# Optimization experiments

Measured on AMD Instinct MI355X. Metric: run time of the kernel, lower is better.

The kernel has to match this reference:

```python
import jax, jax.numpy as jnp
import numpy as np

B, S, DMODEL, HEADS = 2, 2048, 1024, 16
DK = DMODEL // HEADS
DV = DMODEL // HEADS


def setup_inputs() -> dict:
    key = jax.random.key(0)
    kx, kq, kk, kv = jax.random.split(key, 4)
    x = jax.random.normal(kx, (B, S, DMODEL), dtype=jnp.float32)
    # stacked per-head projection weights, shape [H, dmodel, dk/dv]
    # (equivalent to nn.Linear(dmodel, dk, bias=False) per head)
    scale = 1.0 / np.sqrt(DMODEL)
    Wq = jax.random.uniform(kq, (HEADS, DMODEL, DK), jnp.float32, -scale, scale)
    Wk = jax.random.uniform(kk, (HEADS, DMODEL, DK), jnp.float32, -scale, scale)
    Wv = jax.random.uniform(kv, (HEADS, DMODEL, DV), jnp.float32, -scale, scale)
    return {"x": x, "Wq": Wq, "Wk": Wk, "Wv": Wv}


def reference(x, Wq, Wk, Wv):
    # per-head projections, batched across heads: [B,H,S,dk]
    q = jnp.einsum("bsd,hdk->bhsk", x, Wq)
    k = jnp.einsum("bsd,hdk->bhsk", x, Wk)
    v = jnp.einsum("bsd,hdv->bhsv", x, Wv)
    # NOTE: original module applies NO 1/sqrt(dk) scaling — keep faithful
    scores = jnp.einsum("bhqk,bhsk->bhqs", q, k)  # [B,H,S,S]
    attn = jax.nn.softmax(scores, axis=-1)
    out = jnp.einsum("bhqs,bhsv->bhqv", attn, v)  # [B,H,S,dv]
    # concat heads along last dim in head order
    Bsz, H, Sq, Dv = out.shape
    return jnp.transpose(out, (0, 2, 1, 3)).reshape(Bsz, Sq, H * Dv)
```

## Files before the change

### kernel.cpp

```cpp
#include <hip/hip_runtime.h>

#define B_ 2
#define S_ 2048
#define D_ 1024
#define H_ 16
#define DK_ 64
#define M_ (B_ * S_)
#define N_ (3 * D_)

typedef __bf16 bf16x8 __attribute__((ext_vector_type(8)));
typedef short s8vec __attribute__((ext_vector_type(8)));
typedef float f4vec __attribute__((ext_vector_type(4)));

static __device__ __forceinline__ ushort f2b(float f) {
  union { float f; unsigned u; } v; v.f = f;
  unsigned u = v.u;
  u += 0x7FFFu + ((u >> 16) & 1u);
  return (ushort)(u >> 16);
}

static __device__ __forceinline__ unsigned pk2(float a, float b) {
#if __has_builtin(__builtin_amdgcn_cvt_pk_bf16_f32)
  typedef __bf16 b2 __attribute__((ext_vector_type(2)));
  b2 r = __builtin_amdgcn_cvt_pk_bf16_f32(a, b);
  return __builtin_bit_cast(unsigned, r);
#else
  return (unsigned)f2b(a) | ((unsigned)f2b(b) << 16);
#endif
}

static __device__ __forceinline__ float fexp2(float x) {
#if __has_builtin(__builtin_amdgcn_exp2f)
  return __builtin_amdgcn_exp2f(x);
#else
  return exp2f(x);
#endif
}

static __device__ __forceinline__ f4vec mfma16(s8vec a, s8vec b, f4vec c) {
  return __builtin_amdgcn_mfma_f32_16x16x32_bf16(
      __builtin_bit_cast(bf16x8, a), __builtin_bit_cast(bf16x8, b), c, 0, 0, 0);
}

static __device__ __forceinline__ void gl_lds16(const ushort* g, ushort* l) {
  __builtin_amdgcn_global_load_lds(
      (const __attribute__((address_space(1))) unsigned*)g,
      (__attribute__((address_space(3))) unsigned*)l, 16, 0, 0);
}

static __device__ __forceinline__ void wg_barrier_lds() {
  asm volatile("" ::: "memory");
  __builtin_amdgcn_s_waitcnt(0xC07F);
  __builtin_amdgcn_s_barrier();
  asm volatile("" ::: "memory");
}

__global__ void cvt_x(const float* __restrict__ x, ushort* __restrict__ xb) {
  int i = blockIdx.x * 256 + threadIdx.x;
  float4 v = ((const float4*)x)[i];
  ushort4 o;
  o.x = f2b(v.x); o.y = f2b(v.y); o.z = f2b(v.z); o.w = f2b(v.w);
  ((ushort4*)xb)[i] = o;
}

__global__ __launch_bounds__(256) void cvt_w(const float* __restrict__ Wq,
                                             const float* __restrict__ Wk,
                                             const float* __restrict__ Wv,
                                             ushort* __restrict__ wbt) {
  __shared__ ushort T[64 * 72];
  const int w = blockIdx.z, h = blockIdx.y, d0 = blockIdx.x * 64;
  const float* W = (w == 0) ? Wq : (w == 1) ? Wk : Wv;
  const float* src = W + (size_t)h * 65536 + (size_t)d0 * 64;
  const int t = threadIdx.x;
#pragma unroll
  for (int j = 0; j < 4; ++j) {
    int idx = j * 256 + t;
    int dr = idx >> 4, kc = (idx & 15) * 4;
    float4 v = *(const float4*)(src + dr * 64 + kc);
    T[(kc + 0) * 72 + dr] = f2b(v.x);
    T[(kc + 1) * 72 + dr] = f2b(v.y);
    T[(kc + 2) * 72 + dr] = f2b(v.z);
    T[(kc + 3) * 72 + dr] = f2b(v.w);
  }
  __syncthreads();
  const int kk = t >> 2, dcg = (t & 3) * 16;
  ushort* dst = wbt + ((size_t)w * 1024 + h * 64 + kk) * 1024 + d0 + dcg;
  *(s8vec*)dst       = *(const s8vec*)&T[kk * 72 + dcg];
  *(s8vec*)(dst + 8) = *(const s8vec*)&T[kk * 72 + dcg + 8];
}

__global__ __launch_bounds__(256) void proj_gemm(const ushort* __restrict__ xb,
                                                 const ushort* __restrict__ wbt,
                                                 ushort* __restrict__ qkv) {
  __shared__ __attribute__((aligned(16))) ushort As[128 * 64];
  __shared__ __attribute__((aligned(16))) ushort Bs[128 * 64];
  const int tid = threadIdx.x, wid = tid >> 6, lane = tid & 63;
  const int quad = lane >> 4, l15 = lane & 15;
  const int wm = wid & 1, wn = wid >> 1;
  const int m0 = blockIdx.x * 128, n0 = blockIdx.y * 128;

  f4vec acc[4][4];
#pragma unroll
  for (int mb = 0; mb < 4; mb++)
#pragma unroll
    for (int nb = 0; nb < 4; nb++)
#pragma unroll
      for (int i = 0; i < 4; i++) acc[mb][nb][i] = 0.f;

  const int sr = tid >> 3, sg = tid & 7;
  const int lg = sg ^ (sr & 7);
  const ushort* Ab = xb + (size_t)m0 * D_;
  const ushort* Bb = wbt + (size_t)n0 * D_;

  for (int k0 = 0; k0 < D_; k0 += 64) {
    __syncthreads();
#pragma unroll
    for (int j = 0; j < 4; ++j) {
      int r = j * 32 + sr;
      gl_lds16(Ab + (size_t)r * D_ + k0 + lg * 8, &As[j * 2048 + wid * 512]);
      gl_lds16(Bb + (size_t)r * D_ + k0 + lg * 8, &Bs[j * 2048 + wid * 512]);
    }
    __syncthreads();

#pragma unroll
    for (int kb = 0; kb < 2; ++kb) {
      s8vec af[4], bf[4];
#pragma unroll
      for (int mb = 0; mb < 4; ++mb) {
        int m = wm * 64 + mb * 16 + l15;
        int gpos = (kb * 4 + quad) ^ (m & 7);
        af[mb] = *(const s8vec*)&As[m * 64 + gpos * 8];
      }
#pragma unroll
      for (int nb = 0; nb < 4; ++nb) {
        int n = wn * 64 + nb * 16 + l15;
        int gpos = (kb * 4 + quad) ^ (n & 7);
        bf[nb] = *(const s8vec*)&Bs[n * 64 + gpos * 8];
      }
#pragma unroll
      for (int mb = 0; mb < 4; ++mb)
#pragma unroll
        for (int nb = 0; nb < 4; ++nb)
          acc[mb][nb] = mfma16(af[mb], bf[nb], acc[mb][nb]);
    }
  }

  const size_t per = (size_t)B_ * H_ * S_ * DK_;
  const int w = n0 >> 10;
  if (w == 2) {
    ushort* vt = qkv + 2 * per;
#pragma unroll
    for (int mb = 0; mb < 4; ++mb)
#pragma unroll
      for (int nb = 0; nb < 4; ++nb)
#pragma unroll
        for (int i = 0; i < 4; ++i) {
          int m = m0 + wm * 64 + mb * 16 + quad * 4 + i;
          int b = m >> 11, s = m & 2047;
          int n1 = (n0 & 1023) + wn * 64 + nb * 16 + l15;
          vt[((size_t)b * 1024 + n1) * S_ + s] = f2b(acc[mb][nb][i]);
        }
  } else {
    const float qs = (w == 0) ? 1.44269504f : 1.0f;
#pragma unroll
    for (int mb = 0; mb < 4; ++mb)
#pragma unroll
      for (int nb = 0; nb < 4; ++nb)
#pragma unroll
        for (int i = 0; i < 4; ++i) {
          int m = m0 + wm * 64 + mb * 16 + quad * 4 + i;
          int b = m >> 11, s = m & 2047;
          int n1 = (n0 & 1023) + wn * 64 + nb * 16 + l15;
          qkv[(size_t)w * per + (((size_t)b * H_ + (n1 >> 6)) * S_ + s) * 64 + (n1 & 63)] =
              f2b(acc[mb][nb][i] * qs);
        }
  }
}

__global__ __launch_bounds__(256) void attn(const ushort* __restrict__ qg,
                                            const ushort* __restrict__ kg,
                                            const ushort* __restrict__ vtg,
                                            float* __restrict__ out) {
  __shared__ __attribute__((aligned(16))) ushort Ks[128 * 64];
  __shared__ __attribute__((aligned(16))) ushort Vt[2][64 * 64];
  __shared__ __attribute__((aligned(16))) ushort Ps[4][32 * 132];
  const int qt = blockIdx.x, bh = blockIdx.y;
  const int b = bh >> 4, h = bh & 15;
  const int tid = threadIdx.x, wid = tid >> 6, lane = tid & 63;
  const int quad = lane >> 4, l15 = lane & 15, l7 = l15 & 7;

  const ushort* qbase = qg + ((size_t)bh * S_ + qt * 128 + wid * 32) * DK_;
  s8vec aq[2][2];
#pragma unroll
  for (int mb = 0; mb < 2; mb++) {
    aq[mb][0] = *(const s8vec*)(qbase + (size_t)(mb * 16 + l15) * DK_ + quad * 8);
    aq[mb][1] = *(const s8vec*)(qbase + (size_t)(mb * 16 + l15) * DK_ + 32 + quad * 8);
  }

  f4vec o[2][4];
  float lsum[2][4];
#pragma unroll
  for (int mb = 0; mb < 2; mb++)
#pragma unroll
    for (int i = 0; i < 4; i++) {
      lsum[mb][i] = 0.f;
#pragma unroll
      for (int nb = 0; nb < 4; nb++) o[mb][nb][i] = 0.f;
    }

  const int r = tid >> 3, gs = tid & 7;
  const int gk = gs ^ (r & 7);
  const ushort* kb_ = kg + (size_t)bh * S_ * DK_;
  const ushort* vb_ = vtg + (size_t)bh * 64 * S_;

  s8vec kpre[4], vpre[4];
#pragma unroll
  for (int j = 0; j < 4; ++j)
    kpre[j] = *(const s8vec*)(kb_ + (size_t)(j * 32 + r) * DK_ + gk * 8);
  vpre[0] = *(const s8vec*)(vb_ + (size_t)r * S_ + gk * 8);
  vpre[1] = *(const s8vec*)(vb_ + (size_t)r * S_ + 64 + gk * 8);
  vpre[2] = *(const s8vec*)(vb_ + (size_t)(r + 32) * S_ + gk * 8);
  vpre[3] = *(const s8vec*)(vb_ + (size_t)(r + 32) * S_ + 64 + gk * 8);

  for (int kt = 0; kt < S_ / 128; ++kt) {
    wg_barrier_lds();
#pragma unroll
    for (int j = 0; j < 4; ++j)
      *(s8vec*)&Ks[(j * 32 + r) * 64 + gs * 8] = kpre[j];
    *(s8vec*)&Vt[0][r * 64 + gs * 8]        = vpre[0];
    *(s8vec*)&Vt[1][r * 64 + gs * 8]        = vpre[1];
    *(s8vec*)&Vt[0][(r + 32) * 64 + gs * 8] = vpre[2];
    *(s8vec*)&Vt[1][(r + 32) * 64 + gs * 8] = vpre[3];
    if (kt + 1 < S_ / 128) {
      const ushort* kn = kb_ + (size_t)((kt + 1) * 128 + r) * DK_ + gk * 8;
#pragma unroll
      for (int j = 0; j < 4; ++j)
        kpre[j] = *(const s8vec*)(kn + (size_t)(j * 32) * DK_);
      const ushort* vn = vb_ + (size_t)r * S_ + (kt + 1) * 128 + gk * 8;
      vpre[0] = *(const s8vec*)(vn);
      vpre[1] = *(const s8vec*)(vn + 64);
      vpre[2] = *(const s8vec*)(vn + (size_t)32 * S_);
      vpre[3] = *(const s8vec*)(vn + (size_t)32 * S_ + 64);
    }
    wg_barrier_lds();

    f4vec sc[2][8];
#pragma unroll
    for (int nb = 0; nb < 8; nb++) {
      const int row = nb * 16 + l15;
      s8vec bk0 = *(const s8vec*)&Ks[row * 64 + ((0 + quad) ^ l7) * 8];
      s8vec bk1 = *(const s8vec*)&Ks[row * 64 + ((4 + quad) ^ l7) * 8];
#pragma unroll
      for (int mb = 0; mb < 2; mb++) {
        f4vec z;
#pragma unroll
        for (int i = 0; i < 4; i++) z[i] = 0.f;
        z = mfma16(aq[mb][0], bk0, z);
        sc[mb][nb] = mfma16(aq[mb][1], bk1, z);
      }
    }

#pragma unroll
    for (int mb = 0; mb < 2; mb++)
#pragma unroll
      for (int nb = 0; nb < 8; nb++) {
#pragma unroll
        for (int i = 0; i < 4; i++) {
          float p = fexp2(sc[mb][nb][i]);
          sc[mb][nb][i] = p;
          lsum[mb][i] += p;
        }
        unsigned p01 = pk2(sc[mb][nb][0], sc[mb][nb][1]);
        unsigned p23 = pk2(sc[mb][nb][2], sc[mb][nb][3]);
        ushort* pw = &Ps[wid][(mb * 16 + quad * 4) * 132 + nb * 16 + l15];
        pw[0]   = (ushort)p01;
        pw[132] = (ushort)(p01 >> 16);
        pw[264] = (ushort)p23;
        pw[396] = (ushort)(p23 >> 16);
      }

#pragma unroll
    for (int kb2 = 0; kb2 < 4; kb2++) {
      s8vec ap0 = *(const s8vec*)(&Ps[wid][(l15) * 132 + kb2 * 32 + quad * 8]);
      s8vec ap1 = *(const s8vec*)(&Ps[wid][(16 + l15) * 132 + kb2 * 32 + quad * 8]);
      const int half = kb2 >> 1, G = (kb2 & 1) * 4 + quad;
#pragma unroll
      for (int nb = 0; nb < 4; nb++) {
        s8vec bv = *(const s8vec*)&Vt[half][(nb * 16 + l15) * 64 + (G ^ l7) * 8];
        o[0][nb] = mfma16(ap0, bv, o[0][nb]);
        o[1][nb] = mfma16(ap1, bv, o[1][nb]);
      }
    }
  }

#pragma unroll
  for (int mb = 0; mb < 2; mb++)
#pragma unroll
    for (int i = 0; i < 4; i++) {
#pragma unroll
      for (int msk = 1; msk < 16; msk <<= 1)
        lsum[mb][i] += __shfl_xor(lsum[mb][i], msk, 64);
    }

#pragma unroll
  for (int mb = 0; mb < 2; mb++) {
    float* ob = out + ((size_t)b * S_ + qt * 128 + wid * 32 + mb * 16) * D_ + h * DK_;
#pragma unroll
    for (int i = 0; i < 4; i++) {
      float inv = 1.0f / lsum[mb][i];
#pragma unroll
      for (int nb = 0; nb < 4; nb++)
        ob[(size_t)(quad * 4 + i) * D_ + nb * 16 + l15] = o[mb][nb][i] * inv;
    }
  }
}

extern "C" void kernel_launch(void* const* d_in, const int* in_sizes, int n_in,
                              void* d_out, int out_size, void* d_ws, size_t ws_size,
                              hipStream_t stream) {
  const float* x  = (const float*)d_in[0];
  const float* Wq = (const float*)d_in[1];
  const float* Wk = (const float*)d_in[2];
  const float* Wv = (const float*)d_in[3];
  float* out = (float*)d_out;

  ushort* xb  = (ushort*)d_ws;
  ushort* wbt = xb + (size_t)B_ * S_ * D_;
  ushort* qkv = wbt + (size_t)3 * D_ * D_;
  const size_t per = (size_t)B_ * H_ * S_ * DK_;

  cvt_x<<<(B_ * S_ * D_) / 4 / 256, 256, 0, stream>>>(x, xb);
  cvt_w<<<dim3(16, 16, 3), 256, 0, stream>>>(Wq, Wk, Wv, wbt);
  proj_gemm<<<dim3(M_ / 128, N_ / 128), 256, 0, stream>>>(xb, wbt, qkv);
  attn<<<dim3(S_ / 128, B_ * H_), 256, 0, stream>>>(qkv, qkv + per, qkv + 2 * per, out);
}
```

Baseline: 176.9 us.

## Transpose attention MFMA operands, halve KV tile, merge conversion kernels

Merges the x and weight bf16 conversion kernels into one launch to save a kernel launch. In attention, it swaps MFMA operand order so each lane holds a full query row's scores. This turns the row-sum reduction into two shuffles, lets P be written as packed 8-byte swizzled stores without row padding, and lets the output be written as float4. The KV tile shrinks from 128 to 64 keys, which cuts LDS use and registers but doubles the number of loop iterations and barriers.

New measurement: 177.5 us. Within noise of the previous version (+0.4%).

```diff
diff --git a/kernel.cpp b/kernel.cpp
--- a/kernel.cpp
+++ b/kernel.cpp
@@ -55,38 +55,42 @@
   asm volatile("" ::: "memory");
 }
 
-__global__ void cvt_x(const float* __restrict__ x, ushort* __restrict__ xb) {
-  int i = blockIdx.x * 256 + threadIdx.x;
-  float4 v = ((const float4*)x)[i];
-  ushort4 o;
-  o.x = f2b(v.x); o.y = f2b(v.y); o.z = f2b(v.z); o.w = f2b(v.w);
-  ((ushort4*)xb)[i] = o;
-}
-
-__global__ __launch_bounds__(256) void cvt_w(const float* __restrict__ Wq,
-                                             const float* __restrict__ Wk,
-                                             const float* __restrict__ Wv,
-                                             ushort* __restrict__ wbt) {
-  __shared__ ushort T[64 * 72];
-  const int w = blockIdx.z, h = blockIdx.y, d0 = blockIdx.x * 64;
-  const float* W = (w == 0) ? Wq : (w == 1) ? Wk : Wv;
-  const float* src = W + (size_t)h * 65536 + (size_t)d0 * 64;
+__global__ __launch_bounds__(256) void cvt_all(const float* __restrict__ x,
+                                               const float* __restrict__ Wq,
+                                               const float* __restrict__ Wk,
+                                               const float* __restrict__ Wv,
+                                               ushort* __restrict__ xb,
+                                               ushort* __restrict__ wbt) {
   const int t = threadIdx.x;
-#pragma unroll
-  for (int j = 0; j < 4; ++j) {
-    int idx = j * 256 + t;
-    int dr = idx >> 4, kc = (idx & 15) * 4;
-    float4 v = *(const float4*)(src + dr * 64 + kc);
-    T[(kc + 0) * 72 + dr] = f2b(v.x);
-    T[(kc + 1) * 72 + dr] = f2b(v.y);
-    T[(kc + 2) * 72 + dr] = f2b(v.z);
-    T[(kc + 3) * 72 + dr] = f2b(v.w);
-  }
-  __syncthreads();
-  const int kk = t >> 2, dcg = (t & 3) * 16;
-  ushort* dst = wbt + ((size_t)w * 1024 + h * 64 + kk) * 1024 + d0 + dcg;
-  *(s8vec*)dst       = *(const s8vec*)&T[kk * 72 + dcg];
-  *(s8vec*)(dst + 8) = *(const s8vec*)&T[kk * 72 + dcg + 8];
+  if (blockIdx.x < 4096) {
+    int i = blockIdx.x * 256 + t;
+    float4 v = ((const float4*)x)[i];
+    ushort4 o;
+    o.x = f2b(v.x); o.y = f2b(v.y); o.z = f2b(v.z); o.w = f2b(v.w);
+    ((ushort4*)xb)[i] = o;
+  } else {
+    __shared__ ushort T[64 * 72];
+    int bid = blockIdx.x - 4096;
+    int w = bid >> 8, rem = bid & 255;
+    int h = rem >> 4, d0 = (rem & 15) * 64;
+    const float* W = (w == 0) ? Wq : (w == 1) ? Wk : Wv;
+    const float* src = W + (size_t)h * 65536 + (size_t)d0 * 64;
+#pragma unroll
+    for (int j = 0; j < 4; ++j) {
+      int idx = j * 256 + t;
+      int dr = idx >> 4, kc = (idx & 15) * 4;
+      float4 v = *(const float4*)(src + dr * 64 + kc);
+      T[(kc + 0) * 72 + dr] = f2b(v.x);
+      T[(kc + 1) * 72 + dr] = f2b(v.y);
+      T[(kc + 2) * 72 + dr] = f2b(v.z);
+      T[(kc + 3) * 72 + dr] = f2b(v.w);
+    }
+    __syncthreads();
+    const int kk = t >> 2, dcg = (t & 3) * 16;
+    ushort* dst = wbt + ((size_t)w * 1024 + h * 64 + kk) * 1024 + d0 + dcg;
+    *(s8vec*)dst       = *(const s8vec*)&T[kk * 72 + dcg];
+    *(s8vec*)(dst + 8) = *(const s8vec*)&T[kk * 72 + dcg + 8];
+  }
 }
 
 __global__ __launch_bounds__(256) void proj_gemm(const ushort* __restrict__ xb,
@@ -181,9 +185,9 @@
                                             const ushort* __restrict__ kg,
                                             const ushort* __restrict__ vtg,
                                             float* __restrict__ out) {
-  __shared__ __attribute__((aligned(16))) ushort Ks[128 * 64];
-  __shared__ __attribute__((aligned(16))) ushort Vt[2][64 * 64];
-  __shared__ __attribute__((aligned(16))) ushort Ps[4][32 * 132];
+  __shared__ __attribute__((aligned(16))) ushort Ks[64 * 64];
+  __shared__ __attribute__((aligned(16))) ushort Vt[64 * 64];
+  __shared__ __attribute__((aligned(16))) ushort Ps[4][32 * 128];
   const int qt = blockIdx.x, bh = blockIdx.y;
   const int b = bh >> 4, h = bh & 15;
   const int tid = threadIdx.x, wid = tid >> 6, lane = tid & 63;
@@ -198,119 +202,110 @@
   }
 
   f4vec o[2][4];
-  float lsum[2][4];
-#pragma unroll
-  for (int mb = 0; mb < 2; mb++)
-#pragma unroll
-    for (int i = 0; i < 4; i++) {
-      lsum[mb][i] = 0.f;
-#pragma unroll
-      for (int nb = 0; nb < 4; nb++) o[mb][nb][i] = 0.f;
-    }
+  float lsum[2];
+#pragma unroll
+  for (int mb = 0; mb < 2; mb++) {
+    lsum[mb] = 0.f;
+#pragma unroll
+    for (int nb = 0; nb < 4; nb++)
+#pragma unroll
+      for (int i = 0; i < 4; i++) o[mb][nb][i] = 0.f;
+  }
 
   const int r = tid >> 3, gs = tid & 7;
   const int gk = gs ^ (r & 7);
   const ushort* kb_ = kg + (size_t)bh * S_ * DK_;
   const ushort* vb_ = vtg + (size_t)bh * 64 * S_;
 
-  s8vec kpre[4], vpre[4];
-#pragma unroll
-  for (int j = 0; j < 4; ++j)
-    kpre[j] = *(const s8vec*)(kb_ + (size_t)(j * 32 + r) * DK_ + gk * 8);
+  s8vec kpre[2], vpre[2];
+  kpre[0] = *(const s8vec*)(kb_ + (size_t)r * DK_ + gk * 8);
+  kpre[1] = *(const s8vec*)(kb_ + (size_t)(r + 32) * DK_ + gk * 8);
   vpre[0] = *(const s8vec*)(vb_ + (size_t)r * S_ + gk * 8);
-  vpre[1] = *(const s8vec*)(vb_ + (size_t)r * S_ + 64 + gk * 8);
-  vpre[2] = *(const s8vec*)(vb_ + (size_t)(r + 32) * S_ + gk * 8);
-  vpre[3] = *(const s8vec*)(vb_ + (size_t)(r + 32) * S_ + 64 + gk * 8);
-
-  for (int kt = 0; kt < S_ / 128; ++kt) {
+  vpre[1] = *(const s8vec*)(vb_ + (size_t)(r + 32) * S_ + gk * 8);
+
+  for (int kt = 0; kt < S_ / 64; ++kt) {
     wg_barrier_lds();
-#pragma unroll
-    for (int j = 0; j < 4; ++j)
-      *(s8vec*)&Ks[(j * 32 + r) * 64 + gs * 8] = kpre[j];
-    *(s8vec*)&Vt[0][r * 64 + gs * 8]        = vpre[0];
-    *(s8vec*)&Vt[1][r * 64 + gs * 8]        = vpre[1];
-    *(s8vec*)&Vt[0][(r + 32) * 64 + gs * 8] = vpre[2];
-    *(s8vec*)&Vt[1][(r + 32) * 64 + gs * 8] = vpre[3];
-    if (kt + 1 < S_ / 128) {
-      const ushort* kn = kb_ + (size_t)((kt + 1) * 128 + r) * DK_ + gk * 8;
-#pragma unroll
-      for (int j = 0; j < 4; ++j)
-        kpre[j] = *(const s8vec*)(kn + (size_t)(j * 32) * DK_);
-      const ushort* vn = vb_ + (size_t)r * S_ + (kt + 1) * 128 + gk * 8;
+    *(s8vec*)&Ks[r * 64 + gs * 8]        = kpre[0];
+    *(s8vec*)&Ks[(r + 32) * 64 + gs * 8] = kpre[1];
+    *(s8vec*)&Vt[r * 64 + gs * 8]        = vpre[0];
+    *(s8vec*)&Vt[(r + 32) * 64 + gs * 8] = vpre[1];
+    if (kt + 1 < S_ / 64) {
+      const ushort* kn = kb_ + (size_t)((kt + 1) * 64 + r) * DK_ + gk * 8;
+      kpre[0] = *(const s8vec*)(kn);
+      kpre[1] = *(const s8vec*)(kn + (size_t)32 * DK_);
+      const ushort* vn = vb_ + (size_t)r * S_ + (kt + 1) * 64 + gk * 8;
       vpre[0] = *(const s8vec*)(vn);
-      vpre[1] = *(const s8vec*)(vn + 64);
-      vpre[2] = *(const s8vec*)(vn + (size_t)32 * S_);
-      vpre[3] = *(const s8vec*)(vn + (size_t)32 * S_ + 64);
+      vpre[1] = *(const s8vec*)(vn + (size_t)32 * S_);
     }
     wg_barrier_lds();
 
-    f4vec sc[2][8];
-#pragma unroll
-    for (int nb = 0; nb < 8; nb++) {
+    f4vec sct[2][4];
+#pragma unroll
+    for (int nb = 0; nb < 4; nb++) {
       const int row = nb * 16 + l15;
-      s8vec bk0 = *(const s8vec*)&Ks[row * 64 + ((0 + quad) ^ l7) * 8];
-      s8vec bk1 = *(const s8vec*)&Ks[row * 64 + ((4 + quad) ^ l7) * 8];
+      s8vec ak0 = *(const s8vec*)&Ks[row * 64 + ((0 + quad) ^ l7) * 8];
+      s8vec ak1 = *(const s8vec*)&Ks[row * 64 + ((4 + quad) ^ l7) * 8];
 #pragma unroll
       for (int mb = 0; mb < 2; mb++) {
         f4vec z;
 #pragma unroll
         for (int i = 0; i < 4; i++) z[i] = 0.f;
-        z = mfma16(aq[mb][0], bk0, z);
-        sc[mb][nb] = mfma16(aq[mb][1], bk1, z);
-      }
-    }
-
-#pragma unroll
-    for (int mb = 0; mb < 2; mb++)
-#pragma unroll
-      for (int nb = 0; nb < 8; nb++) {
+        z = mfma16(ak0, aq[mb][0], z);
+        sct[mb][nb] = mfma16(ak1, aq[mb][1], z);
+      }
+    }
+
+#pragma unroll
+    for (int mb = 0; mb < 2; mb++) {
+      const int q = mb * 16 + l15;
+#pragma unroll
+      for (int nb = 0; nb < 4; nb++) {
 #pragma unroll
         for (int i = 0; i < 4; i++) {
-          float p = fexp2(sc[mb][nb][i]);
-          sc[mb][nb][i] = p;
-          lsum[mb][i] += p;
+          float p = fexp2(sct[mb][nb][i]);
+          sct[mb][nb][i] = p;
+          lsum[mb] += p;
         }
-        unsigned p01 = pk2(sc[mb][nb][0], sc[mb][nb][1]);
-        unsigned p23 = pk2(sc[mb][nb][2], sc[mb][nb][3]);
-        ushort* pw = &Ps[wid][(mb * 16 + quad * 4) * 132 + nb * 16 + l15];
-        pw[0]   = (ushort)p01;
-        pw[132] = (ushort)(p01 >> 16);
-        pw[264] = (ushort)p23;
-        pw[396] = (ushort)(p23 >> 16);
-      }
-
-#pragma unroll
-    for (int kb2 = 0; kb2 < 4; kb2++) {
-      s8vec ap0 = *(const s8vec*)(&Ps[wid][(l15) * 132 + kb2 * 32 + quad * 8]);
-      s8vec ap1 = *(const s8vec*)(&Ps[wid][(16 + l15) * 132 + kb2 * 32 + quad * 8]);
-      const int half = kb2 >> 1, G = (kb2 & 1) * 4 + quad;
+        unsigned p01 = pk2(sct[mb][nb][0], sct[mb][nb][1]);
+        unsigned p23 = pk2(sct[mb][nb][2], sct[mb][nb][3]);
+        const int c = (nb * 2 + (quad >> 1)) ^ l7;
+        *(uint2*)&Ps[wid][q * 128 + c * 8 + (quad & 1) * 4] = make_uint2(p01, p23);
+      }
+    }
+
+#pragma unroll
+    for (int kc = 0; kc < 2; kc++) {
+      s8vec ap[2];
+#pragma unroll
+      for (int mb = 0; mb < 2; mb++)
+        ap[mb] = *(const s8vec*)&Ps[wid][(mb * 16 + l15) * 128 + (((kc * 4 + quad)) ^ l7) * 8];
 #pragma unroll
       for (int nb = 0; nb < 4; nb++) {
-        s8vec bv = *(const s8vec*)&Vt[half][(nb * 16 + l15) * 64 + (G ^ l7) * 8];
-        o[0][nb] = mfma16(ap0, bv, o[0][nb]);
-        o[1][nb] = mfma16(ap1, bv, o[1][nb]);
-      }
-    }
-  }
-
-#pragma unroll
-  for (int mb = 0; mb < 2; mb++)
-#pragma unroll
-    for (int i = 0; i < 4; i++) {
-#pragma unroll
-      for (int msk = 1; msk < 16; msk <<= 1)
-        lsum[mb][i] += __shfl_xor(lsum[mb][i], msk, 64);
-    }
+        s8vec av = *(const s8vec*)&Vt[(nb * 16 + l15) * 64 + ((kc * 4 + quad) ^ l7) * 8];
+        o[0][nb] = mfma16(av, ap[0], o[0][nb]);
+        o[1][nb] = mfma16(av, ap[1], o[1][nb]);
+      }
+    }
+  }
 
 #pragma unroll
   for (int mb = 0; mb < 2; mb++) {
-    float* ob = out + ((size_t)b * S_ + qt * 128 + wid * 32 + mb * 16) * D_ + h * DK_;
-#pragma unroll
-    for (int i = 0; i < 4; i++) {
-      float inv = 1.0f / lsum[mb][i];
-#pragma unroll
-      for (int nb = 0; nb < 4; nb++)
-        ob[(size_t)(quad * 4 + i) * D_ + nb * 16 + l15] = o[mb][nb][i] * inv;
+    lsum[mb] += __shfl_xor(lsum[mb], 16, 64);
+    lsum[mb] += __shfl_xor(lsum[mb], 32, 64);
+  }
+
+#pragma unroll
+  for (int mb = 0; mb < 2; mb++) {
+    const float inv = 1.0f / lsum[mb];
+    float* ob = out + ((size_t)b * S_ + qt * 128 + wid * 32 + mb * 16 + l15) * D_ + h * DK_;
+#pragma unroll
+    for (int nb = 0; nb < 4; nb++) {
+      float4 v;
+      v.x = o[mb][nb][0] * inv;
+      v.y = o[mb][nb][1] * inv;
+      v.z = o[mb][nb][2] * inv;
+      v.w = o[mb][nb][3] * inv;
+      *(float4*)(ob + nb * 16 + quad * 4) = v;
     }
   }
 }
@@ -329,8 +324,7 @@
   ushort* qkv = wbt + (size_t)3 * D_ * D_;
   const size_t per = (size_t)B_ * H_ * S_ * DK_;
 
-  cvt_x<<<(B_ * S_ * D_) / 4 / 256, 256, 0, stream>>>(x, xb);
-  cvt_w<<<dim3(16, 16, 3), 256, 0, stream>>>(Wq, Wk, Wv, wbt);
+  cvt_all<<<4096 + 768, 256, 0, stream>>>(x, Wq, Wk, Wv, xb, wbt);
   proj_gemm<<<dim3(M_ / 128, N_ / 128), 256, 0, stream>>>(xb, wbt, qkv);
   attn<<<dim3(S_ / 128, B_ * H_), 256, 0, stream>>>(qkv, qkv + per, qkv + 2 * per, out);
 }
```
